# Kernel optimization log

Measured on AMD Instinct MI355X. Metric: run time of the kernel, lower is better.

Reference implementation:

```python
import jax, jax.numpy as jnp
import numpy as np

DFL_CH = 16
NC = 20


def setup_inputs() -> dict:
    key = jax.random.key(0)
    k1, k2, k3, k4, k5 = jax.random.split(key, 5)
    b, h, w, c = 32, 80, 80, 128
    x = jax.random.normal(k1, (b, h, w, c), dtype=jnp.float32)
    w_box = jax.random.normal(k2, (c, 4 * DFL_CH), dtype=jnp.float32) * 0.05
    b_box = jax.random.normal(k3, (4 * DFL_CH,), dtype=jnp.float32) * 0.05
    w_cls = jax.random.normal(k4, (c, NC), dtype=jnp.float32) * 0.05
    b_cls = jax.random.normal(k5, (NC,), dtype=jnp.float32) * 0.05
    return {"x": x, "w_box": w_box, "b_box": b_box, "w_cls": w_cls,
            "b_cls": b_cls, "stride": 8}


def reference(x, w_box, b_box, w_cls, b_cls, stride):
    b, h, w, _ = x.shape
    hw = h * w
    # 1x1 convs == per-pixel matmuls (NHWC)
    box = jnp.einsum('bhwc,co->bhwo', x, w_box) + b_box   # [b,h,w,64]
    cls = jnp.einsum('bhwc,co->bhwo', x, w_cls) + b_cls   # [b,h,w,nc]
    cls_flat = cls.reshape(b, hw, NC)
    # DFL: softmax over 16 bins per coordinate, expectation with weights 0..15
    box_p = box.reshape(b, hw, 4, DFL_CH)
    probs = jax.nn.softmax(box_p, axis=-1)
    bins = jnp.arange(DFL_CH, dtype=x.dtype)
    box_dfl = jnp.einsum('bnfc,c->bnf', probs, bins)       # [b,hw,4]
    # anchor centers (tf.meshgrid default 'xy' indexing)
    s = jnp.asarray(stride, dtype=x.dtype)
    gx = (jnp.arange(w, dtype=x.dtype) + 0.5) * s
    gy = (jnp.arange(h, dtype=x.dtype) + 0.5) * s
    Gx, Gy = jnp.meshgrid(gx, gy)                          # each [h,w]
    anchors = jnp.stack([Gx, Gy], axis=-1).reshape(1, hw, 2)
    a = box_dfl[..., :2]
    bc = box_dfl[..., 2:]
    boxes = jnp.concatenate([(anchors - a + anchors + bc) * 0.5, bc - a], axis=-1)
    return jnp.concatenate([boxes, jax.nn.sigmoid(cls_flat)], axis=-1)
```

## Files before the change

kernel.cpp:

```cpp
#include <hip/hip_runtime.h>


typedef _Float16 half8 __attribute__((ext_vector_type(8)));
typedef __fp16  fp16x2 __attribute__((ext_vector_type(2)));
typedef float f32x4v __attribute__((ext_vector_type(4)));

constexpr int Cc = 128;
constexpr int NPAD = 96;
constexpr int WT_STRIDE = 136;
constexpr int NWAVES = 2048;
constexpr float LOG2E = 1.44269504088896f;

union H8 { half8 h; fp16x2 p[4]; };

__device__ __forceinline__ float sigm(float v) {
    return __builtin_amdgcn_rcpf(1.f + __builtin_amdgcn_exp2f(-LOG2E * v));
}

__global__ __launch_bounds__(256, 2)
void head_kernel(const float* __restrict__ x,
                 const float* __restrict__ w_box,
                 const float* __restrict__ b_box,
                 const float* __restrict__ w_cls,
                 const float* __restrict__ b_cls,
                 const int*   __restrict__ stride_p,
                 float* __restrict__ out)
{
    __shared__ __align__(16) _Float16 Wt[NPAD][WT_STRIDE];
    __shared__ __align__(16) float bias_s[NPAD];
    __shared__ __align__(16) float scdfl[4][16][4];

    const int tid  = threadIdx.x;
    const int wave = tid >> 6;
    const int lane = tid & 63;
    const int c    = lane & 15;
    const int g    = lane >> 4;

    for (int i = tid; i < 128 * 16; i += 256) {
        int k   = i >> 4;
        int ch0 = (i & 15) << 2;
        int f   = ch0 >> 4;
        int b0  = ch0 & 15;
        int R0  = (b0 >> 2) * 16 + (f << 2);
        f32x4v v = *(const f32x4v*)&w_box[k * 64 + ch0];
        Wt[R0 + 0][k] = (_Float16)v[0];
        Wt[R0 + 1][k] = (_Float16)v[1];
        Wt[R0 + 2][k] = (_Float16)v[2];
        Wt[R0 + 3][k] = (_Float16)v[3];
    }
    for (int i = tid; i < 128 * 5; i += 256) {
        int k  = i / 5;
        int c4 = (i - k * 5) << 2;
        f32x4v v = *(const f32x4v*)&w_cls[k * 20 + c4];
        Wt[64 + c4 + 0][k] = (_Float16)v[0];
        Wt[64 + c4 + 1][k] = (_Float16)v[1];
        Wt[64 + c4 + 2][k] = (_Float16)v[2];
        Wt[64 + c4 + 3][k] = (_Float16)v[3];
    }
    for (int i = tid; i < 12 * 128; i += 256) {
        int ch = 84 + (i >> 7);
        int k  = i & 127;
        Wt[ch][k] = (_Float16)0.f;
    }
    if (tid < 64) {
        int f = tid >> 4, b = tid & 15;
        bias_s[(b >> 2) * 16 + (f << 2) + (b & 3)] = b_box[tid];
    } else if (tid < 96) {
        bias_s[tid] = (tid < 84) ? b_cls[tid - 64] : 0.f;
    }
    __syncthreads();

    const float sf = (float)stride_p[0];

    const int wid = blockIdx.x * 4 + wave;
    const int t0 = wid,              t1 = wid + NWAVES;
    const int t2 = wid + 2 * NWAVES, t3 = wid + 3 * NWAVES;
    const int t4 = wid + 4 * NWAVES, t5 = wid + 5 * NWAVES;
    const bool heavy = (wave == (blockIdx.x & 3));
    const int t6 = 6 * NWAVES + blockIdx.x;

    f32x4v xvA[4][2], xvB[4][2], xvC[4][2];

    auto load_tile = [&](f32x4v (&xv)[4][2], int tile) {
        const float* xb = x + (size_t)(tile * 16 + c) * Cc + g * 8;
        #pragma unroll
        for (int ks = 0; ks < 4; ++ks) {
            const float* p = xb + ks * 32;
            xv[ks][0] = *(const f32x4v*)p;
            xv[ks][1] = *(const f32x4v*)(p + 4);
        }
        __builtin_amdgcn_sched_barrier(0);
    };

    auto compute_tile = [&](f32x4v (&xv)[4][2], int tile) {
        f32x4v acc[6];
        #pragma unroll
        for (int nt = 0; nt < 6; ++nt)
            acc[nt] = *(const f32x4v*)&bias_s[nt * 16 + g * 4];

        #pragma unroll
        for (int ks = 0; ks < 4; ++ks) {
            half8 wfrag[6];
            #pragma unroll
            for (int nt = 0; nt < 6; ++nt)
                wfrag[nt] = *(const half8*)&Wt[nt * 16 + c][ks * 32 + g * 8];
            f32x4v lo = xv[ks][0], hi = xv[ks][1];
            H8 bu;
            bu.p[0] = __builtin_amdgcn_cvt_pkrtz(lo[0], lo[1]);
            bu.p[1] = __builtin_amdgcn_cvt_pkrtz(lo[2], lo[3]);
            bu.p[2] = __builtin_amdgcn_cvt_pkrtz(hi[0], hi[1]);
            bu.p[3] = __builtin_amdgcn_cvt_pkrtz(hi[2], hi[3]);
            #pragma unroll
            for (int nt = 0; nt < 6; ++nt)
                acc[nt] = __builtin_amdgcn_mfma_f32_16x16x32_f16(wfrag[nt], bu.h, acc[nt], 0, 0, 0);
        }

        float s = 0.f, ws = 0.f;
        #pragma unroll
        for (int t = 0; t < 4; ++t) {
            f32x4v v = acc[t];
            float e0 = __builtin_amdgcn_exp2f(LOG2E * v[0]);
            float e1 = __builtin_amdgcn_exp2f(LOG2E * v[1]);
            float e2 = __builtin_amdgcn_exp2f(LOG2E * v[2]);
            float e3 = __builtin_amdgcn_exp2f(LOG2E * v[3]);
            s  += e0 + e1 + e2 + e3;
            ws += (float)(4 * t) * e0 + (float)(4 * t + 1) * e1
                + (float)(4 * t + 2) * e2 + (float)(4 * t + 3) * e3;
        }
        const float dfl = ws * __builtin_amdgcn_rcpf(s);

        scdfl[wave][c][g] = dfl;
        f32x4v db = *(const f32x4v*)&scdfl[wave][c][0];

        const int pos0 = (tile % 400) * 16;
        const int yp   = pos0 / 80;
        const int xq   = (pos0 - 80 * yp) + c;
        const float ax = ((float)xq + 0.5f) * sf;
        const float ay = ((float)yp + 0.5f) * sf;
        const float w2 = db[2] - db[0], w3 = db[3] - db[1];

        float* op = out + (size_t)(tile * 16 + c) * 24;

        f32x4v clsA = { sigm(acc[4][0]), sigm(acc[4][1]), sigm(acc[4][2]), sigm(acc[4][3]) };
        *(f32x4v*)(op + 4 + 4 * g) = clsA;
        if (g == 0) {
            f32x4v box = { ax + 0.5f * w2, ay + 0.5f * w3, w2, w3 };
            *(f32x4v*)op = box;
            f32x4v clsB = { sigm(acc[5][0]), sigm(acc[5][1]), sigm(acc[5][2]), sigm(acc[5][3]) };
            *(f32x4v*)(op + 20) = clsB;
        }
    };

    load_tile(xvA, t0);
    load_tile(xvB, t1);
    load_tile(xvC, t2);
    compute_tile(xvA, t0);  load_tile(xvA, t3);
    compute_tile(xvB, t1);  load_tile(xvB, t4);
    compute_tile(xvC, t2);  load_tile(xvC, t5);
    compute_tile(xvA, t3);  if (heavy) load_tile(xvA, t6);
    compute_tile(xvB, t4);
    compute_tile(xvC, t5);
    if (heavy) compute_tile(xvA, t6);
}

extern "C" void kernel_launch(void* const* d_in, const int* in_sizes, int n_in,
                              void* d_out, int out_size, void* d_ws, size_t ws_size,
                              hipStream_t stream) {
    const float* x      = (const float*)d_in[0];
    const float* w_box  = (const float*)d_in[1];
    const float* b_box  = (const float*)d_in[2];
    const float* w_cls  = (const float*)d_in[3];
    const float* b_cls  = (const float*)d_in[4];
    const int*   stride_p = (const int*)d_in[5];
    float* out = (float*)d_out;

    dim3 grid(512), block(256);
    hipLaunchKernelGGL(head_kernel, grid, block, 0, stream,
                       x, w_box, b_box, w_cls, b_cls, stride_p, out);
}
```

Measured before the change: 28.36 us.

## Hoist weight fragments into registers and overlap x prefetch with weight staging

Issues the first two x tile loads before staging weights into LDS, so global load latency overlaps with weight conversion. The weight transpose now uses vectorized half4 LDS stores, and zero-padding uses 16-byte stores. All 24 weight fragments are loaded once into registers instead of re-read from LDS on every tile. The prefetch depth drops from three buffers to two and launch bounds allow one block per SIMD group, trading occupancy and in-flight loads for higher register use.

Result: faster. 26.91 us, median of 2 (-5.1%).

```diff
diff --git a/kernel.cpp b/kernel.cpp
--- a/kernel.cpp
+++ b/kernel.cpp
@@ -2,6 +2,7 @@
 
 
 typedef _Float16 half8 __attribute__((ext_vector_type(8)));
+typedef _Float16 half4 __attribute__((ext_vector_type(4)));
 typedef __fp16  fp16x2 __attribute__((ext_vector_type(2)));
 typedef float f32x4v __attribute__((ext_vector_type(4)));
 
@@ -17,7 +18,7 @@
     return __builtin_amdgcn_rcpf(1.f + __builtin_amdgcn_exp2f(-LOG2E * v));
 }
 
-__global__ __launch_bounds__(256, 2)
+__global__ __launch_bounds__(256, 1)
 void head_kernel(const float* __restrict__ x,
                  const float* __restrict__ w_box,
                  const float* __restrict__ b_box,
@@ -36,42 +37,6 @@
     const int c    = lane & 15;
     const int g    = lane >> 4;
 
-    for (int i = tid; i < 128 * 16; i += 256) {
-        int k   = i >> 4;
-        int ch0 = (i & 15) << 2;
-        int f   = ch0 >> 4;
-        int b0  = ch0 & 15;
-        int R0  = (b0 >> 2) * 16 + (f << 2);
-        f32x4v v = *(const f32x4v*)&w_box[k * 64 + ch0];
-        Wt[R0 + 0][k] = (_Float16)v[0];
-        Wt[R0 + 1][k] = (_Float16)v[1];
-        Wt[R0 + 2][k] = (_Float16)v[2];
-        Wt[R0 + 3][k] = (_Float16)v[3];
-    }
-    for (int i = tid; i < 128 * 5; i += 256) {
-        int k  = i / 5;
-        int c4 = (i - k * 5) << 2;
-        f32x4v v = *(const f32x4v*)&w_cls[k * 20 + c4];
-        Wt[64 + c4 + 0][k] = (_Float16)v[0];
-        Wt[64 + c4 + 1][k] = (_Float16)v[1];
-        Wt[64 + c4 + 2][k] = (_Float16)v[2];
-        Wt[64 + c4 + 3][k] = (_Float16)v[3];
-    }
-    for (int i = tid; i < 12 * 128; i += 256) {
-        int ch = 84 + (i >> 7);
-        int k  = i & 127;
-        Wt[ch][k] = (_Float16)0.f;
-    }
-    if (tid < 64) {
-        int f = tid >> 4, b = tid & 15;
-        bias_s[(b >> 2) * 16 + (f << 2) + (b & 3)] = b_box[tid];
-    } else if (tid < 96) {
-        bias_s[tid] = (tid < 84) ? b_cls[tid - 64] : 0.f;
-    }
-    __syncthreads();
-
-    const float sf = (float)stride_p[0];
-
     const int wid = blockIdx.x * 4 + wave;
     const int t0 = wid,              t1 = wid + NWAVES;
     const int t2 = wid + 2 * NWAVES, t3 = wid + 3 * NWAVES;
@@ -79,7 +44,7 @@
     const bool heavy = (wave == (blockIdx.x & 3));
     const int t6 = 6 * NWAVES + blockIdx.x;
 
-    f32x4v xvA[4][2], xvB[4][2], xvC[4][2];
+    f32x4v xvA[4][2], xvB[4][2];
 
     auto load_tile = [&](f32x4v (&xv)[4][2], int tile) {
         const float* xb = x + (size_t)(tile * 16 + c) * Cc + g * 8;
@@ -92,6 +57,60 @@
         __builtin_amdgcn_sched_barrier(0);
     };
 
+    load_tile(xvA, t0);
+    load_tile(xvB, t1);
+
+    for (int i = tid; i < 512; i += 256) {
+        int ch0 = (i >> 5) << 2;
+        int k0  = (i & 31) << 2;
+        int f   = ch0 >> 4;
+        int b0  = ch0 & 15;
+        int R0  = (b0 >> 2) * 16 + (f << 2);
+        f32x4v v0 = *(const f32x4v*)&w_box[(k0 + 0) * 64 + ch0];
+        f32x4v v1 = *(const f32x4v*)&w_box[(k0 + 1) * 64 + ch0];
+        f32x4v v2 = *(const f32x4v*)&w_box[(k0 + 2) * 64 + ch0];
+        f32x4v v3 = *(const f32x4v*)&w_box[(k0 + 3) * 64 + ch0];
+        #pragma unroll
+        for (int r = 0; r < 4; ++r) {
+            half4 h = { (_Float16)v0[r], (_Float16)v1[r], (_Float16)v2[r], (_Float16)v3[r] };
+            *(half4*)&Wt[R0 + r][k0] = h;
+        }
+    }
+    for (int i = tid; i < 160; i += 256) {
+        int ch0 = (i / 32) << 2;
+        int k0  = (i & 31) << 2;
+        f32x4v v0 = *(const f32x4v*)&w_cls[(k0 + 0) * 20 + ch0];
+        f32x4v v1 = *(const f32x4v*)&w_cls[(k0 + 1) * 20 + ch0];
+        f32x4v v2 = *(const f32x4v*)&w_cls[(k0 + 2) * 20 + ch0];
+        f32x4v v3 = *(const f32x4v*)&w_cls[(k0 + 3) * 20 + ch0];
+        #pragma unroll
+        for (int r = 0; r < 4; ++r) {
+            half4 h = { (_Float16)v0[r], (_Float16)v1[r], (_Float16)v2[r], (_Float16)v3[r] };
+            *(half4*)&Wt[64 + ch0 + r][k0] = h;
+        }
+    }
+    for (int i = tid; i < 12 * 16; i += 256) {
+        int ch = 84 + (i >> 4);
+        int k0 = (i & 15) << 3;
+        *(f32x4v*)&Wt[ch][k0] = (f32x4v){0.f, 0.f, 0.f, 0.f};
+    }
+    if (tid < 64) {
+        int f = tid >> 4, b = tid & 15;
+        bias_s[(b >> 2) * 16 + (f << 2) + (b & 3)] = b_box[tid];
+    } else if (tid < 96) {
+        bias_s[tid] = (tid < 84) ? b_cls[tid - 64] : 0.f;
+    }
+    __syncthreads();
+
+    half8 wf[4][6];
+    #pragma unroll
+    for (int ks = 0; ks < 4; ++ks)
+        #pragma unroll
+        for (int nt = 0; nt < 6; ++nt)
+            wf[ks][nt] = *(const half8*)&Wt[nt * 16 + c][ks * 32 + g * 8];
+
+    const float sf = (float)stride_p[0];
+
     auto compute_tile = [&](f32x4v (&xv)[4][2], int tile) {
         f32x4v acc[6];
         #pragma unroll
@@ -100,10 +119,6 @@
 
         #pragma unroll
         for (int ks = 0; ks < 4; ++ks) {
-            half8 wfrag[6];
-            #pragma unroll
-            for (int nt = 0; nt < 6; ++nt)
-                wfrag[nt] = *(const half8*)&Wt[nt * 16 + c][ks * 32 + g * 8];
             f32x4v lo = xv[ks][0], hi = xv[ks][1];
             H8 bu;
             bu.p[0] = __builtin_amdgcn_cvt_pkrtz(lo[0], lo[1]);
@@ -112,7 +127,7 @@
             bu.p[3] = __builtin_amdgcn_cvt_pkrtz(hi[2], hi[3]);
             #pragma unroll
             for (int nt = 0; nt < 6; ++nt)
-                acc[nt] = __builtin_amdgcn_mfma_f32_16x16x32_f16(wfrag[nt], bu.h, acc[nt], 0, 0, 0);
+                acc[nt] = __builtin_amdgcn_mfma_f32_16x16x32_f16(wf[ks][nt], bu.h, acc[nt], 0, 0, 0);
         }
 
         float s = 0.f, ws = 0.f;
@@ -151,15 +166,12 @@
         }
     };
 
-    load_tile(xvA, t0);
-    load_tile(xvB, t1);
-    load_tile(xvC, t2);
-    compute_tile(xvA, t0);  load_tile(xvA, t3);
-    compute_tile(xvB, t1);  load_tile(xvB, t4);
-    compute_tile(xvC, t2);  load_tile(xvC, t5);
-    compute_tile(xvA, t3);  if (heavy) load_tile(xvA, t6);
-    compute_tile(xvB, t4);
-    compute_tile(xvC, t5);
+    compute_tile(xvA, t0);  load_tile(xvA, t2);
+    compute_tile(xvB, t1);  load_tile(xvB, t3);
+    compute_tile(xvA, t2);  load_tile(xvA, t4);
+    compute_tile(xvB, t3);  load_tile(xvB, t5);
+    compute_tile(xvA, t4);  if (heavy) load_tile(xvA, t6);
+    compute_tile(xvB, t5);
     if (heavy) compute_tile(xvA, t6);
 }
 
```
